# Optimization experiments

Hardware: AMD Instinct MI355X
Metric: run time of the kernel (lower is better)

The kernel has to match this reference:

```python
import jax, jax.numpy as jnp
import numpy as np

NUM_HEADS = 12
ALPHA = 4.0
EPS = 1e-6

def safe_pow(x, p):
    # relu(x)**p with grad-safe handling of x<=0 (avoids nan from log(0) in pow grads)
    xp = jnp.where(x > 0, x, 1.0)
    return jnp.where(x > 0, xp ** p, 0.0)

def setup_inputs() -> dict:
    key = jax.random.key(0)
    ks = jax.random.split(key, 9)
    B, N, C = 8, 4096, 768
    Hn, hd, ksz = NUM_HEADS, C // NUM_HEADS, 5
    return {
        "x": jax.random.normal(ks[0], (B, N, C), jnp.float32),
        "Wqg": jax.random.normal(ks[1], (C, 2 * C), jnp.float32) * 0.02,
        "Wkv": jax.random.normal(ks[2], (C, 2 * C), jnp.float32) * 0.02,
        "Wproj": jax.random.normal(ks[3], (C, C), jnp.float32) * 0.02,
        "bproj": jnp.zeros((C,), jnp.float32),
        "dwc_w": jax.random.normal(ks[4], (hd, 1, ksz, ksz), jnp.float32) * 0.05,
        "dwc_b": jnp.zeros((hd,), jnp.float32),
        "power_p": jax.random.normal(ks[5], (1, Hn, 1, hd), jnp.float32) * 0.01,
        "scale_p": jax.random.normal(ks[6], (1, 1, C), jnp.float32) * 0.01,
        "pos_enc": jax.random.normal(ks[7], (1, N, C), jnp.float32) * 0.01,
    }

def reference(x, Wqg, Wkv, Wproj, bproj, dwc_w, dwc_b, power_p, scale_p, pos_enc):
    B, N, C = x.shape
    Hn = NUM_HEADS
    hd = C // Hn
    # q/g projection: [B,N,2C] -> q = [...,0,:], g = [...,1,:]
    qg = (x @ Wqg).reshape(B, N, 2, C)
    q, g = qg[:, :, 0], qg[:, :, 1]
    # k/v projection (sr_ratio == 1)
    kvp = x @ Wkv
    k, v = kvp[..., :C], kvp[..., C:]
    k = k + pos_enc
    scale = jax.nn.softplus(scale_p)            # [1,1,C]
    power = 1.0 + ALPHA * jax.nn.sigmoid(power_p)  # [1,Hn,1,hd]
    q = q / scale
    k = k / scale
    # -> [B,Hn,N,hd]
    q = q.reshape(B, N, Hn, hd).transpose(0, 2, 1, 3)
    k = k.reshape(B, N, Hn, hd).transpose(0, 2, 1, 3)
    v = v.reshape(B, N, Hn, hd).transpose(0, 2, 1, 3)
    q_pos = safe_pow(q, power)
    q_neg = safe_pow(-q, power)
    k_pos = safe_pow(k, power)
    k_neg = safe_pow(-k, power)
    q_sim = jnp.concatenate([q_pos, q_neg], -1)  # [B,Hn,N,2hd]
    q_opp = jnp.concatenate([q_neg, q_pos], -1)
    k_cat = jnp.concatenate([k_pos, k_neg], -1)
    v1, v2 = jnp.split(v, 2, axis=-1)            # [B,Hn,N,hd/2]
    n = N
    inv_n = 1.0 / n
    k_mean = k_cat.mean(axis=2, keepdims=True)   # [B,Hn,1,2hd]
    z_sim = 1.0 / (jnp.einsum('bhnk,bhmk->bhnm', q_sim, k_mean) + EPS)  # [B,Hn,N,1]
    kv1 = jnp.einsum('bhnk,bhnv->bhkv', k_cat, v1) * inv_n
    x_sim = jnp.einsum('bhnk,bhkv->bhnv', q_sim, kv1) * z_sim
    z_opp = 1.0 / (jnp.einsum('bhnk,bhmk->bhnm', q_opp, k_mean) + EPS)
    kv2 = jnp.einsum('bhnk,bhnv->bhkv', k_cat, v2) * inv_n
    x_opp = jnp.einsum('bhnk,bhkv->bhnv', q_opp, kv2) * z_opp
    xa = jnp.concatenate([x_sim, x_opp], -1).transpose(0, 2, 1, 3).reshape(B, N, C)
    # depthwise-conv positional branch on v (head-major channel layout)
    Hs = int(np.sqrt(N))
    v_img = v.reshape(B * Hn, Hs, Hs, hd).transpose(0, 3, 1, 2)  # [B*Hn, hd, Hs, Hs]
    v_conv = jax.lax.conv_general_dilated(
        v_img, dwc_w, (1, 1), 'SAME', feature_group_count=hd,
        dimension_numbers=('NCHW', 'OIHW', 'NCHW')) + dwc_b[None, :, None, None]
    v_pos = v_conv.reshape(B, C, N).transpose(0, 2, 1)  # [B,N,C]
    out = (xa + v_pos) * g
    return out @ Wproj + bproj
```

## Files before the change

kernel.cpp:

```cpp
#include <hip/hip_runtime.h>


typedef _Float16 f16;
typedef __attribute__((ext_vector_type(4))) float f32x4;
typedef __attribute__((ext_vector_type(8))) _Float16 f16x8;
typedef __attribute__((ext_vector_type(4))) _Float16 f16x4;

__device__ __forceinline__ void mfma(f32x4& c, f16x8 a, f16x8 b) {
  c = __builtin_amdgcn_mfma_f32_16x16x32_f16(a, b, c, 0, 0, 0);
}

__device__ __forceinline__ void gload_lds16(const f16* g, f16* l) {
  __builtin_amdgcn_global_load_lds(
      (__attribute__((address_space(1))) void*)g,
      (__attribute__((address_space(3))) void*)l, 16, 0, 0);
}

__device__ __forceinline__ f16x8 relu8(f16x8 v) {
  f16x8 r;
#pragma unroll
  for (int u = 0; u < 8; ++u) r[u] = (v[u] > (f16)0) ? v[u] : (f16)0;
  return r;
}
__device__ __forceinline__ f16x8 nrelu8(f16x8 v) {
  f16x8 r;
#pragma unroll
  for (int u = 0; u < 8; ++u) r[u] = (v[u] < (f16)0) ? (f16)(-v[u]) : (f16)0;
  return r;
}

__global__ void prep_scalars_kernel(const float* __restrict__ scale_p,
                                    const float* __restrict__ power_p,
                                    float* __restrict__ iscale,
                                    float* __restrict__ powr) {
  int c = blockIdx.x * 256 + threadIdx.x;
  if (c < 768) {
    float sp = scale_p[c];
    float s = (sp > 20.f) ? sp : log1pf(__expf(sp));
    iscale[c] = 1.f / s;
    powr[c] = 1.f + 4.f / (1.f + __expf(-power_p[c]));
  }
}

__global__ __launch_bounds__(256) void cast_x_kernel(const float* __restrict__ x,
                                                     f16* __restrict__ xblk) {
  __shared__ f16 tile[128 * 72];
  const int kb = blockIdx.x, mt = blockIdx.y, t = threadIdx.x;
  const float* xp = x + (size_t)mt * 128 * 768 + kb * 64;
#pragma unroll
  for (int it = 0; it < 8; ++it) {
    int idx = it * 256 + t;
    int row = idx >> 4, kc4 = (idx & 15) * 4;
    f32x4 v = *(const f32x4*)(xp + (size_t)row * 768 + kc4);
    f16x4 h;
    h[0] = (f16)v[0]; h[1] = (f16)v[1]; h[2] = (f16)v[2]; h[3] = (f16)v[3];
    *(f16x4*)(tile + row * 72 + kc4) = h;
  }
  __syncthreads();
  f16* op = xblk + (size_t)mt * 98304 + kb * 8192;
#pragma unroll
  for (int it = 0; it < 4; ++it) {
    int c = it * 256 + t;
    int kchunk = c >> 7, m = c & 127;
    f16x4 lo = *(const f16x4*)(tile + m * 72 + kchunk * 8);
    f16x4 hi = *(const f16x4*)(tile + m * 72 + kchunk * 8 + 4);
    *(f16x4*)(op + c * 8) = lo;
    *(f16x4*)(op + c * 8 + 4) = hi;
  }
}

__global__ __launch_bounds__(256) void transpose_w_kernel(const float* __restrict__ W,
                                                          f16* __restrict__ outblk,
                                                          int Cc, int col_off) {
  __shared__ float tile[32][33];
  const int c0 = blockIdx.x * 32, r0 = blockIdx.y * 32, t = threadIdx.x;
#pragma unroll
  for (int it = 0; it < 4; ++it) {
    int rr = it * 8 + (t >> 5), cc = t & 31;
    tile[rr][cc] = W[(size_t)(r0 + rr) * Cc + c0 + cc];
  }
  __syncthreads();
  if (t < 128) {
    int cl = t >> 2, rb = t & 3;
    int cg = col_off + c0 + cl;
    int rg = r0 + rb * 8;
    f16x4 v0, v1;
#pragma unroll
    for (int u = 0; u < 4; ++u) v0[u] = (f16)tile[rb * 8 + u][cl];
#pragma unroll
    for (int u = 0; u < 4; ++u) v1[u] = (f16)tile[rb * 8 + 4 + u][cl];
    size_t base = (size_t)(cg >> 7) * 98304 + (size_t)(rg >> 3) * 1024 +
                  (size_t)(cg & 127) * 8;
    *(f16x4*)(outblk + base) = v0;
    *(f16x4*)(outblk + base + 4) = v1;
  }
}

template <int MODE>
__global__ __launch_bounds__(512, 4) void gemm_kernel(
    const f16* __restrict__ Ablk, const f16* __restrict__ Bblk,
    const float* __restrict__ powr, const float* __restrict__ iscale,
    const float* __restrict__ pos_enc, const float* __restrict__ bproj,
    f16* __restrict__ qpow, f16* __restrict__ gbuf, f16* __restrict__ kpow,
    f16* __restrict__ vt, float* __restrict__ outp) {
  constexpr int A_SZ = 4096;
  constexpr int STR  = 12288;
  __shared__ f16 smem[3 * STR];
  const int t = threadIdx.x;
  const int wid = t >> 6, lane = t & 63;
  const int c16 = lane & 15, q = lane >> 4;
  const int ntile = blockIdx.x, mtile = blockIdx.y;
  const int wm = wid >> 2, wn = wid & 3;
  const int bh2 = wn >> 1, bc = (wn & 1) * 64;
  const f16* Ap = Ablk + (size_t)mtile * 98304;
  const f16* Bp = Bblk + (size_t)ntile * 196608;

  auto STAGE = [&](int buf, int k0) {
    const size_t gk = (size_t)(k0 >> 3) * 1024;
    gload_lds16(Ap + gk + (size_t)t * 8, smem + buf * STR + wid * 512);
    gload_lds16(Bp + gk + (size_t)t * 8, smem + buf * STR + A_SZ + wid * 512);
    gload_lds16(Bp + 98304 + gk + (size_t)t * 8,
                smem + buf * STR + A_SZ + 4096 + wid * 512);
  };

  f32x4 acc[4][4];
#pragma unroll
  for (int i = 0; i < 4; ++i)
#pragma unroll
    for (int j = 0; j < 4; ++j) acc[i][j] = (f32x4){0.f, 0.f, 0.f, 0.f};

  STAGE(0, 0);
  STAGE(1, 32);
  asm volatile("s_waitcnt vmcnt(3)");
  __builtin_amdgcn_sched_barrier(0);
  __builtin_amdgcn_s_barrier();
  __builtin_amdgcn_sched_barrier(0);

  int cur = 0, nx2 = 2;
  for (int j = 0; j < 24; ++j) {
    if (j < 22) STAGE(nx2, (j + 2) * 32);
    const f16* A_ = smem + cur * STR;
    const f16* B_ = smem + cur * STR + A_SZ + bh2 * 4096;
    f16x8 af[4], bf[4];
    const int kc = q * 1024;
#pragma unroll
    for (int mi = 0; mi < 4; ++mi)
      af[mi] = *(const f16x8*)(A_ + kc + (wm * 64 + mi * 16 + c16) * 8);
#pragma unroll
    for (int ni = 0; ni < 4; ++ni)
      bf[ni] = *(const f16x8*)(B_ + kc + (bc + ni * 16 + c16) * 8);
    asm volatile("s_waitcnt lgkmcnt(0)");
    __builtin_amdgcn_sched_barrier(0);
    __builtin_amdgcn_s_setprio(1);
#pragma unroll
    for (int mi = 0; mi < 4; ++mi)
#pragma unroll
      for (int ni = 0; ni < 4; ++ni) mfma(acc[mi][ni], af[mi], bf[ni]);
    __builtin_amdgcn_s_setprio(0);
    __builtin_amdgcn_sched_barrier(0);
    if (j < 22)       asm volatile("s_waitcnt vmcnt(3)");
    else if (j == 22) asm volatile("s_waitcnt vmcnt(0)");
    __builtin_amdgcn_sched_barrier(0);
    __builtin_amdgcn_s_barrier();
    __builtin_amdgcn_sched_barrier(0);
    cur = (cur == 2) ? 0 : cur + 1;
    nx2 = (nx2 == 2) ? 0 : nx2 + 1;
  }

  if (MODE == 0) {
    const int sec = ntile / 3;
    const int csb = (ntile - sec * 3) * 256;
    const int b = mtile >> 5;
    const int nim0 = (mtile & 31) * 128;
#pragma unroll
    for (int mi = 0; mi < 4; ++mi) {
      const int nloc = nim0 + wm * 64 + mi * 16 + q * 4;
#pragma unroll
      for (int ni = 0; ni < 4; ++ni) {
        const int cs = csb + wn * 64 + ni * 16 + c16;
        const int h = cs >> 6, d = cs & 63;
        const int bh = b * 12 + h;
        if (sec == 0) {
          const float p = powr[cs], isc = iscale[cs];
          const size_t qb2 = (size_t)bh * 262144 + (size_t)(nloc >> 7) * 8192;
          const int dpo = (d >> 3) * 1024 + (d & 7);
#pragma unroll
          for (int r2 = 0; r2 < 4; ++r2) {
            float val = acc[mi][ni][r2] * isc;
            float av = fabsf(val);
            float e = (av > 0.f) ? exp2f(p * __log2f(av)) : 0.f;
            float s = (val > 0.f) ? e : ((val < 0.f) ? -e : 0.f);
            int mrow = (nloc + r2) & 127;
            qpow[qb2 + mrow * 8 + dpo] = (f16)s;
          }
        } else if (sec == 1) {
#pragma unroll
          for (int r2 = 0; r2 < 4; ++r2) {
            const int tok = b * 4096 + nloc + r2;
            gbuf[(size_t)(tok >> 7) * 98304 + (size_t)(cs >> 3) * 1024 +
                 (tok & 127) * 8 + (cs & 7)] = (f16)acc[mi][ni][r2];
          }
        } else if (sec == 2) {
          const float p = powr[cs], isc = iscale[cs];
          f16x4 pk;
#pragma unroll
          for (int r2 = 0; r2 < 4; ++r2) {
            int n = nloc + r2;
            float val = (acc[mi][ni][r2] + pos_enc[(size_t)n * 768 + cs]) * isc;
            float av = fabsf(val);
            float e = (av > 0.f) ? exp2f(p * __log2f(av)) : 0.f;
            pk[r2] = (f16)((val > 0.f) ? e : ((val < 0.f) ? -e : 0.f));
          }
          const size_t kb2 =
              (size_t)bh * 262144 + (size_t)(nloc >> 3) * 512 + (nloc & 7);
          *(f16x4*)(kpow + kb2 + (size_t)d * 8) = pk;
        } else {
          f16x4 vv4;
#pragma unroll
          for (int r2 = 0; r2 < 4; ++r2) vv4[r2] = (f16)acc[mi][ni][r2];
          *(f16x4*)(vt + (size_t)(bh * 64 + d) * 4096 + nloc) = vv4;
        }
      }
    }
  } else {
#pragma unroll
    for (int mi = 0; mi < 4; ++mi) {
      const int tok0 = mtile * 128 + wm * 64 + mi * 16 + q * 4;
#pragma unroll
      for (int ni = 0; ni < 4; ++ni) {
        const int col = ntile * 256 + wn * 64 + ni * 16 + c16;
        const float bb = bproj[col];
#pragma unroll
        for (int r2 = 0; r2 < 4; ++r2)
          outp[(size_t)(tok0 + r2) * 768 + col] = acc[mi][ni][r2] + bb;
      }
    }
  }
}

__global__ __launch_bounds__(256) void kv_kernel(const f16* __restrict__ kpow,
                                                 const f16* __restrict__ vt,
                                                 float* __restrict__ kvp,
                                                 float* __restrict__ ksp) {
  __shared__ f16 Ks[8192];
  __shared__ f16 Vs[4096];
  __shared__ float rp[256], rn[256];
  const int bh = blockIdx.x, split = blockIdx.y, t = threadIdx.x;
  const int wave = t >> 6, lane = t & 63;
  const int c16 = lane & 15, q = lane >> 4;
  const f16* kb = kpow + (size_t)bh * 262144;
  const f16* vb = vt + (size_t)bh * 64 * 4096;
  f32x4 acc[4][2];
#pragma unroll
  for (int i = 0; i < 4; ++i)
#pragma unroll
    for (int j = 0; j < 2; ++j) acc[i][j] = (f32x4){0.f, 0.f, 0.f, 0.f};
  float sp = 0.f, sn = 0.f;

  const int n_beg = split * 1024, n_end = n_beg + 1024;
  for (int n0 = n_beg; n0 < n_end; n0 += 64) {
    f16x8 kr[2], vr[2];
#pragma unroll
    for (int r = 0; r < 2; ++r)
      kr[r] = *(const f16x8*)(kb + (size_t)n0 * 64 + (size_t)(r * 256 + t) * 8);
#pragma unroll
    for (int r = 0; r < 2; ++r) {
      int cc = r * 256 + t;
      int vv = cc >> 3, nc = cc & 7;
      vr[r] = *(const f16x8*)(vb + (size_t)vv * 4096 + n0 + nc * 8);
    }
#pragma unroll
    for (int r = 0; r < 2; ++r)
#pragma unroll
      for (int u = 0; u < 8; ++u) {
        float f = (float)kr[r][u];
        sp += (f > 0.f) ? f : 0.f;
        sn += (f < 0.f) ? -f : 0.f;
      }
    __syncthreads();
#pragma unroll
    for (int r = 0; r < 2; ++r) {
      int cp = r * 256 + t;
      int nch = cp >> 6, d = cp & 63;
      *(f16x8*)(Ks + (size_t)(nch * 1024 + d * 8)) = relu8(kr[r]);
      *(f16x8*)(Ks + (size_t)(nch * 1024 + (d + 64) * 8)) = nrelu8(kr[r]);
    }
#pragma unroll
    for (int r = 0; r < 2; ++r) {
      int cc = r * 256 + t;
      int vv = cc >> 3, nc = cc & 7;
      *(f16x8*)(Vs + (size_t)(nc * 64 + (vv ^ nc)) * 8) = vr[r];
    }
    __syncthreads();
#pragma unroll
    for (int s = 0; s < 2; ++s) {
      f16x8 af[4], bf2[2];
#pragma unroll
      for (int i = 0; i < 4; ++i) {
        int m = i * 16 + c16, nc2 = s * 4 + q;
        af[i] = *(const f16x8*)(Vs + (nc2 * 64 + (m ^ nc2)) * 8);
      }
#pragma unroll
      for (int j = 0; j < 2; ++j)
        bf2[j] = *(const f16x8*)(Ks + ((s * 4 + q) * 128 + wave * 32 + j * 16 + c16) * 8);
#pragma unroll
      for (int i = 0; i < 4; ++i)
#pragma unroll
        for (int j = 0; j < 2; ++j) mfma(acc[i][j], af[i], bf2[j]);
    }
    __syncthreads();
  }
  float* kvb = kvp + (size_t)(bh * 4 + split) * 8192;
#pragma unroll
  for (int i = 0; i < 4; ++i)
#pragma unroll
    for (int j = 0; j < 2; ++j) {
      int kk = wave * 32 + j * 16 + c16;
      int vv0 = i * 16 + q * 4;
#pragma unroll
      for (int r2 = 0; r2 < 4; ++r2)
        kvb[(size_t)(vv0 + r2) * 128 + kk] = acc[i][j][r2];
    }
  rp[t] = sp; rn[t] = sn;
  __syncthreads();
  if (t < 64) {
    float* ko = ksp + (size_t)(bh * 4 + split) * 128;
    ko[t] = rp[t] + rp[t + 64] + rp[t + 128] + rp[t + 192];
    ko[64 + t] = rn[t] + rn[t + 64] + rn[t + 128] + rn[t + 192];
  }
}

__global__ void bx_kernel(const float* __restrict__ kvp,
                          const float* __restrict__ ksp, f16* __restrict__ bxt) {
  const int bh = blockIdx.x, kk = threadIdx.x;
  const float inv_n = 1.f / 4096.f;
  const float* kv0 = kvp + (size_t)bh * 4 * 8192;
  const float* ks0 = ksp + (size_t)bh * 4 * 128;
  f16* ob = bxt + (size_t)bh * 80 * 128;
  for (int nn = 0; nn < 32; ++nn) {
    float v = kv0[nn * 128 + kk] + kv0[8192 + nn * 128 + kk] +
              kv0[16384 + nn * 128 + kk] + kv0[24576 + nn * 128 + kk];
    ob[nn * 128 + kk] = (f16)(v * inv_n);
  }
  const int kx = kk ^ 64;
  for (int nn = 32; nn < 64; ++nn) {
    float v = kv0[nn * 128 + kx] + kv0[8192 + nn * 128 + kx] +
              kv0[16384 + nn * 128 + kx] + kv0[24576 + nn * 128 + kx];
    ob[nn * 128 + kk] = (f16)(v * inv_n);
  }
  float s0 = ks0[kk] + ks0[128 + kk] + ks0[256 + kk] + ks0[384 + kk];
  ob[64 * 128 + kk] = (f16)(s0 * inv_n);
  float s1 = ks0[kx] + ks0[128 + kx] + ks0[256 + kx] + ks0[384 + kx];
  ob[65 * 128 + kk] = (f16)(s1 * inv_n);
  for (int nn = 66; nn < 80; ++nn) ob[nn * 128 + kk] = (f16)0.f;
}

__global__ __launch_bounds__(256) void conv_kernel(const f16* __restrict__ vt,
                                                   const float* __restrict__ w,
                                                   const float* __restrict__ bias,
                                                   f16* __restrict__ vpos) {
  __shared__ float img[68 * 69];
  const int blk = blockIdx.x;
  const int d = blk & 63, bh = blk >> 6;
  const f16* src = vt + (size_t)(bh * 64 + d) * 4096;
  for (int i = threadIdx.x; i < 68 * 16; i += 256) {
    int yy = i >> 4, g4 = i & 15;
    int y = yy - 2;
    float v0 = 0.f, v1 = 0.f, v2 = 0.f, v3 = 0.f;
    if ((unsigned)y < 64u) {
      f16x4 v = *(const f16x4*)(src + y * 64 + g4 * 4);
      v0 = (float)v[0]; v1 = (float)v[1]; v2 = (float)v[2]; v3 = (float)v[3];
    }
    float* row = img + yy * 69 + 2 + g4 * 4;
    row[0] = v0; row[1] = v1; row[2] = v2; row[3] = v3;
  }
  for (int i = threadIdx.x; i < 68 * 4; i += 256) {
    int yy = i >> 2, c = i & 3;
    int xx = (c < 2) ? c : 64 + c;
    img[yy * 69 + xx] = 0.f;
  }
  float wr[25];
#pragma unroll
  for (int k = 0; k < 25; ++k) wr[k] = w[d * 25 + k];
  const float bb = bias[d];
  __syncthreads();
  f16* dst = vpos + (size_t)(bh * 64 + d) * 4096;
  for (int g4 = threadIdx.x; g4 < 1024; g4 += 256) {
    int y = g4 >> 4, x4 = (g4 & 15) * 4;
    float o0 = bb, o1 = bb, o2 = bb, o3 = bb;
#pragma unroll
    for (int ky = 0; ky < 5; ++ky) {
      const float* row = img + (y + ky) * 69 + x4;
      float r[8];
#pragma unroll
      for (int u = 0; u < 8; ++u) r[u] = row[u];
#pragma unroll
      for (int kx = 0; kx < 5; ++kx) {
        float wv = wr[ky * 5 + kx];
        o0 += r[kx] * wv;
        o1 += r[kx + 1] * wv;
        o2 += r[kx + 2] * wv;
        o3 += r[kx + 3] * wv;
      }
    }
    f16x4 st;
    st[0] = (f16)o0; st[1] = (f16)o1; st[2] = (f16)o2; st[3] = (f16)o3;
    *(f16x4*)(dst + y * 64 + x4) = st;
  }
}

__global__ __launch_bounds__(256) void xa_kernel(
    const f16* __restrict__ qpow, const f16* __restrict__ bxt,
    const f16* __restrict__ vpos, const f16* __restrict__ gbuf,
    f16* __restrict__ pre) {
  __shared__ f16 Qs[16384];
  __shared__ f16 Ps[64 * 134];
  __shared__ float zs[256];
  const int nb = blockIdx.x, bh = blockIdx.y;
  const int b = bh / 12, h = bh % 12;
  const int t = threadIdx.x;
  const int wave = t >> 6, lane = t & 63;
  const int c16 = lane & 15, q = lane >> 4;
  const f16* qb = qpow + (size_t)bh * 262144 + (size_t)nb * 8192;
  const size_t gp2 = (size_t)(b * 32 + nb) * 98304 + (size_t)(h * 8) * 1024;
  f16x8 qr[4], gr[4];
#pragma unroll
  for (int r = 0; r < 4; ++r)
    qr[r] = *(const f16x8*)(qb + (size_t)(r * 256 + t) * 8);
#pragma unroll
  for (int r = 0; r < 4; ++r)
    gr[r] = *(const f16x8*)(gbuf + gp2 + (size_t)(r * 256 + t) * 8);
#pragma unroll
  for (int r = 0; r < 4; ++r) {
    int c = r * 256 + t;
    int dch = c >> 7, row = c & 127;
    *(f16x8*)(Qs + (size_t)(dch * 1024 + row * 8)) = relu8(qr[r]);
    *(f16x8*)(Qs + (size_t)((dch + 8) * 1024 + row * 8)) = nrelu8(qr[r]);
  }
  {
    const f16* vpb = vpos + (size_t)bh * 262144 + (size_t)nb * 128;
#pragma unroll
    for (int it = 0; it < 4; ++it) {
      int idx = it * 256 + t;
      int col = idx >> 4, nc = idx & 15;
      f16x8 v = *(const f16x8*)(vpb + (size_t)col * 4096 + nc * 8);
      *(f16x8*)(Ps + col * 134 + nc * 8) = v;
    }
  }
  __syncthreads();
  f32x4 acc[2][5];
#pragma unroll
  for (int i = 0; i < 2; ++i)
#pragma unroll
    for (int j = 0; j < 5; ++j) acc[i][j] = (f32x4){0.f, 0.f, 0.f, 0.f};
  const f16* bx = bxt + (size_t)bh * 80 * 128;
#pragma unroll
  for (int s = 0; s < 4; ++s) {
    f16x8 af[2], bf5[5];
#pragma unroll
    for (int i = 0; i < 2; ++i)
      af[i] = *(const f16x8*)(Qs + ((s * 4 + q) * 1024 + (wave * 32 + i * 16 + c16) * 8));
#pragma unroll
    for (int j = 0; j < 5; ++j)
      bf5[j] = *(const f16x8*)(bx + (size_t)(j * 16 + c16) * 128 + s * 32 + q * 8);
#pragma unroll
    for (int i = 0; i < 2; ++i)
#pragma unroll
      for (int j = 0; j < 5; ++j) mfma(acc[i][j], af[i], bf5[j]);
  }
  if (c16 < 2) {
#pragma unroll
    for (int i = 0; i < 2; ++i) {
      int mloc = wave * 32 + i * 16 + q * 4;
#pragma unroll
      for (int r2 = 0; r2 < 4; ++r2) zs[(mloc + r2) * 2 + c16] = acc[i][4][r2];
    }
  }
  __syncthreads();
  f16* Gs = Qs;
  f16* Os = Qs + 8192;
#pragma unroll
  for (int r = 0; r < 4; ++r)
    *(f16x8*)(Gs + (size_t)(r * 256 + t) * 8) = gr[r];
  __syncthreads();
#pragma unroll
  for (int i = 0; i < 2; ++i) {
    const int mbase = wave * 32 + i * 16 + q * 4;
#pragma unroll
    for (int j = 0; j < 4; ++j) {
      const int col = j * 16 + c16;
      const int zsel = col >> 5;
      const int gidx = (col >> 3) * 1024 + (col & 7);
#pragma unroll
      for (int r2 = 0; r2 < 4; ++r2) {
        const int mloc = mbase + r2;
        const float den = zs[mloc * 2 + zsel];
        const float xav = acc[i][j][r2] / (den + 1e-6f);
        const float vp = (float)Ps[col * 134 + mloc];
        const float gg = (float)Gs[gidx + mloc * 8];
        Os[gidx + mloc * 8] = (f16)((xav + vp) * gg);
      }
    }
  }
  __syncthreads();
#pragma unroll
  for (int r = 0; r < 4; ++r)
    *(f16x8*)(pre + gp2 + (size_t)(r * 256 + t) * 8) =
        *(const f16x8*)(Os + (size_t)(r * 256 + t) * 8);
}

extern "C" void kernel_launch(void* const* d_in, const int* in_sizes, int n_in,
                              void* d_out, int out_size, void* d_ws, size_t ws_size,
                              hipStream_t stream) {
  const float* x       = (const float*)d_in[0];
  const float* Wqg     = (const float*)d_in[1];
  const float* Wkv     = (const float*)d_in[2];
  const float* Wproj   = (const float*)d_in[3];
  const float* bproj   = (const float*)d_in[4];
  const float* dwc_w   = (const float*)d_in[5];
  const float* dwc_b   = (const float*)d_in[6];
  const float* power_p = (const float*)d_in[7];
  const float* scale_p = (const float*)d_in[8];
  const float* pos_enc = (const float*)d_in[9];
  float* outp = (float*)d_out;

  char* ws = (char*)d_ws;
  constexpr size_t o_qpow = 0;
  constexpr size_t o_kpow = 50331648;
  constexpr size_t o_vt   = 100663296;
  constexpr size_t o_gbuf = 150994944;
  constexpr size_t o_xblk = 201326592;
  constexpr size_t o_wta  = 251658240;
  constexpr size_t o_wtp  = 256376832;
  constexpr size_t o_isc  = 257556480;
  constexpr size_t o_pwr  = 257560576;
  constexpr size_t o_bxt  = 257564672;

  f16*   qpow = (f16*)(ws + o_qpow);
  f16*   kpow = (f16*)(ws + o_kpow);
  f16*   vt   = (f16*)(ws + o_vt);
  f16*   gbuf = (f16*)(ws + o_gbuf);
  f16*   xblk = (f16*)(ws + o_xblk);
  f16*   wta  = (f16*)(ws + o_wta);
  f16*   wtp  = (f16*)(ws + o_wtp);
  float* isc  = (float*)(ws + o_isc);
  float* pwr  = (float*)(ws + o_pwr);
  f16*   bxt  = (f16*)(ws + o_bxt);
  float* kvp  = (float*)(ws + o_xblk);
  float* ksp  = (float*)(ws + o_xblk + 12582912);
  f16*   vpos = kpow;
  f16*   pre  = xblk;

  prep_scalars_kernel<<<dim3(3), 256, 0, stream>>>(scale_p, power_p, isc, pwr);
  cast_x_kernel<<<dim3(12, 256), 256, 0, stream>>>(x, xblk);
  transpose_w_kernel<<<dim3(48, 24), 256, 0, stream>>>(Wqg, wta, 1536, 0);
  transpose_w_kernel<<<dim3(48, 24), 256, 0, stream>>>(Wkv, wta, 1536, 1536);
  transpose_w_kernel<<<dim3(24, 24), 256, 0, stream>>>(Wproj, wtp, 768, 0);
  gemm_kernel<0><<<dim3(12, 256), 512, 0, stream>>>(
      xblk, wta, pwr, isc, pos_enc, nullptr, qpow, gbuf, kpow, vt, nullptr);
  kv_kernel<<<dim3(96, 4), 256, 0, stream>>>(kpow, vt, kvp, ksp);
  bx_kernel<<<96, 128, 0, stream>>>(kvp, ksp, bxt);
  conv_kernel<<<6144, 256, 0, stream>>>(vt, dwc_w, dwc_b, vpos);
  xa_kernel<<<dim3(32, 96), 256, 0, stream>>>(qpow, bxt, vpos, gbuf, pre);
  gemm_kernel<1><<<dim3(3, 256), 512, 0, stream>>>(
      pre, wtp, nullptr, nullptr, nullptr, bproj, nullptr, nullptr, nullptr,
      nullptr, outp);
}
```

Baseline: 590.5 us.

## Retile GEMM to 256x128 blocks with 4 waves and register double-buffered fragments

The GEMM block tile moves from 128x256 with 8 waves to 256x128 with 4 waves, so each wave now computes a 128x64 sub-tile (8x4 MFMA accumulators). LDS fragment reads are double-buffered in registers, so the reads for the next k-step are issued before the MFMAs of the current one. The aim is more MFMA work per LDS read and better overlap of LDS latency with compute. In exchange the kernel needs more registers, which lowers occupancy, and the grid dimensions and epilogue index mappings change for both GEMM launches.

```diff
diff --git a/kernel.cpp b/kernel.cpp
--- a/kernel.cpp
+++ b/kernel.cpp
@@ -97,84 +97,105 @@
 }
 
 template <int MODE>
-__global__ __launch_bounds__(512, 4) void gemm_kernel(
+__global__ __launch_bounds__(256, 2) void gemm_kernel(
     const f16* __restrict__ Ablk, const f16* __restrict__ Bblk,
     const float* __restrict__ powr, const float* __restrict__ iscale,
     const float* __restrict__ pos_enc, const float* __restrict__ bproj,
     f16* __restrict__ qpow, f16* __restrict__ gbuf, f16* __restrict__ kpow,
     f16* __restrict__ vt, float* __restrict__ outp) {
-  constexpr int A_SZ = 4096;
-  constexpr int STR  = 12288;
+  constexpr int STR = 12288;
   __shared__ f16 smem[3 * STR];
   const int t = threadIdx.x;
   const int wid = t >> 6, lane = t & 63;
   const int c16 = lane & 15, q = lane >> 4;
   const int ntile = blockIdx.x, mtile = blockIdx.y;
-  const int wm = wid >> 2, wn = wid & 3;
-  const int bh2 = wn >> 1, bc = (wn & 1) * 64;
-  const f16* Ap = Ablk + (size_t)mtile * 98304;
-  const f16* Bp = Bblk + (size_t)ntile * 196608;
+  const int wm = wid >> 1, wn = wid & 1;
+  const f16* Ap = Ablk + (size_t)mtile * 196608;
+  const f16* Bp = Bblk + (size_t)ntile * 98304;
 
   auto STAGE = [&](int buf, int k0) {
-    const size_t gk = (size_t)(k0 >> 3) * 1024;
-    gload_lds16(Ap + gk + (size_t)t * 8, smem + buf * STR + wid * 512);
-    gload_lds16(Bp + gk + (size_t)t * 8, smem + buf * STR + A_SZ + wid * 512);
-    gload_lds16(Bp + 98304 + gk + (size_t)t * 8,
-                smem + buf * STR + A_SZ + 4096 + wid * 512);
+    const size_t gk = (size_t)k0 * 128;
+    f16* ldsb = smem + buf * STR;
+#pragma unroll
+    for (int r = 0; r < 4; ++r)
+      gload_lds16(Ap + (size_t)((t >> 7) * 98304) + gk + r * 1024 + (t & 127) * 8,
+                  ldsb + r * 2048 + wid * 512);
+#pragma unroll
+    for (int r = 0; r < 2; ++r)
+      gload_lds16(Bp + gk + r * 2048 + (size_t)t * 8,
+                  ldsb + 8192 + r * 2048 + wid * 512);
   };
-
-  f32x4 acc[4][4];
-#pragma unroll
-  for (int i = 0; i < 4; ++i)
+  auto READF = [&](int buf, f16x8* af, f16x8* bf) {
+    const f16* A_ = smem + buf * STR + q * 2048;
+    const f16* B_ = smem + buf * STR + 8192 + q * 1024;
+#pragma unroll
+    for (int mi = 0; mi < 8; ++mi)
+      af[mi] = *(const f16x8*)(A_ + (wm * 128 + mi * 16 + c16) * 8);
+#pragma unroll
+    for (int ni = 0; ni < 4; ++ni)
+      bf[ni] = *(const f16x8*)(B_ + (wn * 64 + ni * 16 + c16) * 8);
+  };
+
+  f32x4 acc[8][4];
+#pragma unroll
+  for (int i = 0; i < 8; ++i)
 #pragma unroll
     for (int j = 0; j < 4; ++j) acc[i][j] = (f32x4){0.f, 0.f, 0.f, 0.f};
+
+  f16x8 afA[8], bfA[4], afB[8], bfB[4];
 
   STAGE(0, 0);
   STAGE(1, 32);
-  asm volatile("s_waitcnt vmcnt(3)");
+  asm volatile("s_waitcnt vmcnt(6)");
   __builtin_amdgcn_sched_barrier(0);
   __builtin_amdgcn_s_barrier();
   __builtin_amdgcn_sched_barrier(0);
-
-  int cur = 0, nx2 = 2;
-  for (int j = 0; j < 24; ++j) {
-    if (j < 22) STAGE(nx2, (j + 2) * 32);
-    const f16* A_ = smem + cur * STR;
-    const f16* B_ = smem + cur * STR + A_SZ + bh2 * 4096;
-    f16x8 af[4], bf[4];
-    const int kc = q * 1024;
-#pragma unroll
-    for (int mi = 0; mi < 4; ++mi)
-      af[mi] = *(const f16x8*)(A_ + kc + (wm * 64 + mi * 16 + c16) * 8);
-#pragma unroll
-    for (int ni = 0; ni < 4; ++ni)
-      bf[ni] = *(const f16x8*)(B_ + kc + (bc + ni * 16 + c16) * 8);
+  READF(0, afA, bfA);
+
+  int cur = 0, nxt = 1, nn = 2;
+#pragma unroll 1
+  for (int jj = 0; jj < 12; ++jj) {
+    const int j0 = 2 * jj, j1 = j0 + 1;
+    if (j0 < 22) STAGE(nn, (j0 + 2) * 32);
+    if (j0 < 22) asm volatile("s_waitcnt vmcnt(6)");
+    else         asm volatile("s_waitcnt vmcnt(0)");
     asm volatile("s_waitcnt lgkmcnt(0)");
-    __builtin_amdgcn_sched_barrier(0);
-    __builtin_amdgcn_s_setprio(1);
-#pragma unroll
-    for (int mi = 0; mi < 4; ++mi)
-#pragma unroll
-      for (int ni = 0; ni < 4; ++ni) mfma(acc[mi][ni], af[mi], bf[ni]);
-    __builtin_amdgcn_s_setprio(0);
-    __builtin_amdgcn_sched_barrier(0);
-    if (j < 22)       asm volatile("s_waitcnt vmcnt(3)");
-    else if (j == 22) asm volatile("s_waitcnt vmcnt(0)");
     __builtin_amdgcn_sched_barrier(0);
     __builtin_amdgcn_s_barrier();
     __builtin_amdgcn_sched_barrier(0);
-    cur = (cur == 2) ? 0 : cur + 1;
-    nx2 = (nx2 == 2) ? 0 : nx2 + 1;
+    READF(nxt, afB, bfB);
+    __builtin_amdgcn_s_setprio(1);
+#pragma unroll
+    for (int mi = 0; mi < 8; ++mi)
+#pragma unroll
+      for (int ni = 0; ni < 4; ++ni) mfma(acc[mi][ni], afA[mi], bfA[ni]);
+    __builtin_amdgcn_s_setprio(0);
+    { int tmp = cur; cur = nxt; nxt = nn; nn = tmp; }
+    if (j1 < 22) STAGE(nn, (j1 + 2) * 32);
+    if (j1 < 22) asm volatile("s_waitcnt vmcnt(6)");
+    else         asm volatile("s_waitcnt vmcnt(0)");
+    asm volatile("s_waitcnt lgkmcnt(0)");
+    __builtin_amdgcn_sched_barrier(0);
+    __builtin_amdgcn_s_barrier();
+    __builtin_amdgcn_sched_barrier(0);
+    if (j1 < 23) READF(nxt, afA, bfA);
+    __builtin_amdgcn_s_setprio(1);
+#pragma unroll
+    for (int mi = 0; mi < 8; ++mi)
+#pragma unroll
+      for (int ni = 0; ni < 4; ++ni) mfma(acc[mi][ni], afB[mi], bfB[ni]);
+    __builtin_amdgcn_s_setprio(0);
+    { int tmp = cur; cur = nxt; nxt = nn; nn = tmp; }
   }
 
   if (MODE == 0) {
-    const int sec = ntile / 3;
-    const int csb = (ntile - sec * 3) * 256;
-    const int b = mtile >> 5;
-    const int nim0 = (mtile & 31) * 128;
-#pragma unroll
-    for (int mi = 0; mi < 4; ++mi) {
-      const int nloc = nim0 + wm * 64 + mi * 16 + q * 4;
+    const int sec = ntile / 6;
+    const int csb = (ntile - sec * 6) * 128;
+    const int b = mtile >> 4;
+    const int nim0 = (mtile & 15) * 256;
+#pragma unroll
+    for (int mi = 0; mi < 8; ++mi) {
+      const int nloc = nim0 + wm * 128 + mi * 16 + q * 4;
 #pragma unroll
       for (int ni = 0; ni < 4; ++ni) {
         const int cs = csb + wn * 64 + ni * 16 + c16;
@@ -224,11 +245,11 @@
     }
   } else {
 #pragma unroll
-    for (int mi = 0; mi < 4; ++mi) {
-      const int tok0 = mtile * 128 + wm * 64 + mi * 16 + q * 4;
+    for (int mi = 0; mi < 8; ++mi) {
+      const int tok0 = mtile * 256 + wm * 128 + mi * 16 + q * 4;
 #pragma unroll
       for (int ni = 0; ni < 4; ++ni) {
-        const int col = ntile * 256 + wn * 64 + ni * 16 + c16;
+        const int col = ntile * 128 + wn * 64 + ni * 16 + c16;
         const float bb = bproj[col];
 #pragma unroll
         for (int r2 = 0; r2 < 4; ++r2)
@@ -556,13 +577,13 @@
   transpose_w_kernel<<<dim3(48, 24), 256, 0, stream>>>(Wqg, wta, 1536, 0);
   transpose_w_kernel<<<dim3(48, 24), 256, 0, stream>>>(Wkv, wta, 1536, 1536);
   transpose_w_kernel<<<dim3(24, 24), 256, 0, stream>>>(Wproj, wtp, 768, 0);
-  gemm_kernel<0><<<dim3(12, 256), 512, 0, stream>>>(
+  gemm_kernel<0><<<dim3(24, 128), 256, 0, stream>>>(
       xblk, wta, pwr, isc, pos_enc, nullptr, qpow, gbuf, kpow, vt, nullptr);
   kv_kernel<<<dim3(96, 4), 256, 0, stream>>>(kpow, vt, kvp, ksp);
   bx_kernel<<<96, 128, 0, stream>>>(kvp, ksp, bxt);
   conv_kernel<<<6144, 256, 0, stream>>>(vt, dwc_w, dwc_b, vpos);
   xa_kernel<<<dim3(32, 96), 256, 0, stream>>>(qpow, bxt, vpos, gbuf, pre);
-  gemm_kernel<1><<<dim3(3, 256), 512, 0, stream>>>(
+  gemm_kernel<1><<<dim3(6, 128), 256, 0, stream>>>(
       pre, wtp, nullptr, nullptr, nullptr, bproj, nullptr, nullptr, nullptr,
       nullptr, outp);
 }
```

Result: slower. 603.6 us (+2.2%).

## Load GEMM B operand directly into registers with double buffering, stage only A in LDS

Applied to the files above, without the earlier changes.

The GEMM main loop no longer stages the B tile through shared memory. Each wave loads its B fragments straight from global memory into registers, double-buffered across iterations, while A is still staged in LDS through a triple buffer. LDS use drops from 12288 to 4096 halves per stage, which lowers LDS traffic and footprint. In exchange, B fragments are fetched redundantly by waves that share them, adds register pressure, and relies on hand-tuned vmcnt counts for correctness.

```diff
diff --git a/kernel.cpp b/kernel.cpp
--- a/kernel.cpp
+++ b/kernel.cpp
@@ -103,8 +103,7 @@
     const float* __restrict__ pos_enc, const float* __restrict__ bproj,
     f16* __restrict__ qpow, f16* __restrict__ gbuf, f16* __restrict__ kpow,
     f16* __restrict__ vt, float* __restrict__ outp) {
-  constexpr int A_SZ = 4096;
-  constexpr int STR  = 12288;
+  constexpr int STR = 4096;
   __shared__ f16 smem[3 * STR];
   const int t = threadIdx.x;
   const int wid = t >> 6, lane = t & 63;
@@ -114,14 +113,17 @@
   const int bh2 = wn >> 1, bc = (wn & 1) * 64;
   const f16* Ap = Ablk + (size_t)mtile * 98304;
   const f16* Bp = Bblk + (size_t)ntile * 196608;
-
-  auto STAGE = [&](int buf, int k0) {
-    const size_t gk = (size_t)(k0 >> 3) * 1024;
-    gload_lds16(Ap + gk + (size_t)t * 8, smem + buf * STR + wid * 512);
-    gload_lds16(Bp + gk + (size_t)t * 8, smem + buf * STR + A_SZ + wid * 512);
-    gload_lds16(Bp + 98304 + gk + (size_t)t * 8,
-                smem + buf * STR + A_SZ + 4096 + wid * 512);
+  const f16* Bl = Bp + (size_t)bh2 * 98304 + q * 1024 + (bc + c16) * 8;
+
+  auto STAGE_A = [&](int buf, int k0) {
+    gload_lds16(Ap + (size_t)(k0 >> 3) * 1024 + (size_t)t * 8,
+                smem + buf * STR + (size_t)t * 8);
   };
+  auto LOADB = [&](f16x8* bf, int k0) {
+    const f16* bp = Bl + (size_t)(k0 >> 3) * 1024;
+#pragma unroll
+    for (int ni = 0; ni < 4; ++ni) bf[ni] = *(const f16x8*)(bp + ni * 128);
+  };
 
   f32x4 acc[4][4];
 #pragma unroll
@@ -129,42 +131,66 @@
 #pragma unroll
     for (int j = 0; j < 4; ++j) acc[i][j] = (f32x4){0.f, 0.f, 0.f, 0.f};
 
-  STAGE(0, 0);
-  STAGE(1, 32);
-  asm volatile("s_waitcnt vmcnt(3)");
+  f16x8 bfA[4], bfB[4];
+
+  STAGE_A(0, 0);
+  LOADB(bfA, 0);
+  STAGE_A(1, 32);
+  asm volatile("s_waitcnt vmcnt(1)");
   __builtin_amdgcn_sched_barrier(0);
   __builtin_amdgcn_s_barrier();
   __builtin_amdgcn_sched_barrier(0);
 
-  int cur = 0, nx2 = 2;
-  for (int j = 0; j < 24; ++j) {
-    if (j < 22) STAGE(nx2, (j + 2) * 32);
-    const f16* A_ = smem + cur * STR;
-    const f16* B_ = smem + cur * STR + A_SZ + bh2 * 4096;
-    f16x8 af[4], bf[4];
-    const int kc = q * 1024;
-#pragma unroll
-    for (int mi = 0; mi < 4; ++mi)
-      af[mi] = *(const f16x8*)(A_ + kc + (wm * 64 + mi * 16 + c16) * 8);
-#pragma unroll
-    for (int ni = 0; ni < 4; ++ni)
-      bf[ni] = *(const f16x8*)(B_ + kc + (bc + ni * 16 + c16) * 8);
-    asm volatile("s_waitcnt lgkmcnt(0)");
-    __builtin_amdgcn_sched_barrier(0);
-    __builtin_amdgcn_s_setprio(1);
-#pragma unroll
-    for (int mi = 0; mi < 4; ++mi)
-#pragma unroll
-      for (int ni = 0; ni < 4; ++ni) mfma(acc[mi][ni], af[mi], bf[ni]);
-    __builtin_amdgcn_s_setprio(0);
-    __builtin_amdgcn_sched_barrier(0);
-    if (j < 22)       asm volatile("s_waitcnt vmcnt(3)");
-    else if (j == 22) asm volatile("s_waitcnt vmcnt(0)");
+  int cur = 0, nn = 2;
+#pragma unroll 1
+  for (int jj = 0; jj < 12; ++jj) {
+    const int j0 = jj * 2, j1 = j0 + 1;
+    if (j0 < 22) STAGE_A(nn, (j0 + 2) * 32);
+    LOADB(bfB, j1 * 32);
+    {
+      const f16* A_ = smem + cur * STR + q * 1024;
+      f16x8 af[4];
+#pragma unroll
+      for (int mi = 0; mi < 4; ++mi)
+        af[mi] = *(const f16x8*)(A_ + (wm * 64 + mi * 16 + c16) * 8);
+      __builtin_amdgcn_s_setprio(1);
+#pragma unroll
+      for (int mi = 0; mi < 4; ++mi)
+#pragma unroll
+        for (int ni = 0; ni < 4; ++ni) mfma(acc[mi][ni], af[mi], bfA[ni]);
+      __builtin_amdgcn_s_setprio(0);
+    }
+    if (j0 < 22) asm volatile("s_waitcnt vmcnt(5)");
+    else         asm volatile("s_waitcnt vmcnt(4)");
     __builtin_amdgcn_sched_barrier(0);
     __builtin_amdgcn_s_barrier();
     __builtin_amdgcn_sched_barrier(0);
     cur = (cur == 2) ? 0 : cur + 1;
-    nx2 = (nx2 == 2) ? 0 : nx2 + 1;
+    nn = (nn == 2) ? 0 : nn + 1;
+    if (j1 < 22) STAGE_A(nn, (j1 + 2) * 32);
+    if (j1 < 23) LOADB(bfA, (j1 + 1) * 32);
+    {
+      const f16* A_ = smem + cur * STR + q * 1024;
+      f16x8 af[4];
+#pragma unroll
+      for (int mi = 0; mi < 4; ++mi)
+        af[mi] = *(const f16x8*)(A_ + (wm * 64 + mi * 16 + c16) * 8);
+      __builtin_amdgcn_s_setprio(1);
+#pragma unroll
+      for (int mi = 0; mi < 4; ++mi)
+#pragma unroll
+        for (int ni = 0; ni < 4; ++ni) mfma(acc[mi][ni], af[mi], bfB[ni]);
+      __builtin_amdgcn_s_setprio(0);
+    }
+    if (j1 < 23) {
+      if (j1 < 22) asm volatile("s_waitcnt vmcnt(5)");
+      else         asm volatile("s_waitcnt vmcnt(4)");
+      __builtin_amdgcn_sched_barrier(0);
+      __builtin_amdgcn_s_barrier();
+      __builtin_amdgcn_sched_barrier(0);
+    }
+    cur = (cur == 2) ? 0 : cur + 1;
+    nn = (nn == 2) ? 0 : nn + 1;
   }
 
   if (MODE == 0) {
```

Result: slower. 613.2 us (+3.8%).
